# Optimization experiments

Measured on AMD Instinct MI355X. Metric: run time of the kernel, lower is better.

## Reference

```python
import jax, jax.numpy as jnp
import numpy as np

B, N, D_IN, D_HID, D_OUT = 8, 512, 4608, 4608, 1152
DROP = 0.1
INV_SQRT2 = 0.7071067811865476
INV_SQRT_2PI = 0.3989422804014327


def _clean(s):
    # nan -> 1e-5, inf -> 1.0 (matches torch.where chain)
    return jnp.where(jnp.isnan(s), jnp.asarray(1e-5, s.dtype),
                     jnp.where(jnp.isinf(s), jnp.asarray(1.0, s.dtype), s))


def kl_regularizer(w_mu, w_sigma):
    d = w_mu.shape[0]
    ws = jax.nn.softplus(w_sigma)  # log(1+exp(w_sigma))
    return 0.5 * jnp.mean(d * ws + jnp.sum(w_mu * w_mu, axis=0) - d - d * jnp.log(ws))


def vdp_linear(mu_in, Sigma_in, w_mu, w_sigma):
    mu_out = jnp.matmul(mu_in, w_mu)                                 # [B,N,U]
    kl = kl_regularizer(w_mu, w_sigma)
    W_Sigma = jax.nn.softplus(w_sigma)                               # [U]
    Sigma_1 = jnp.matmul(Sigma_in, w_mu * w_mu)                      # w^T Sigma_in w (diag)
    Sigma_2 = jnp.sum(mu_in * mu_in, axis=-1, keepdims=True) * W_Sigma
    Sigma_3 = jnp.sum(Sigma_in, axis=-1, keepdims=True) * W_Sigma
    return mu_out, _clean(Sigma_1 + Sigma_2 + Sigma_3), kl


def vdp_gelu(mu_in, Sigma_in):
    # exact (erf) gelu and its analytic derivative: Phi(x) + x*phi(x)
    cdf = 0.5 * (1.0 + jax.lax.erf(mu_in * INV_SQRT2))
    pdf = jnp.exp(-0.5 * mu_in * mu_in) * INV_SQRT_2PI
    grad = cdf + mu_in * pdf
    return mu_in * cdf, grad * grad * Sigma_in


def vdp_dropout(mu_in, Sigma_in, mask):
    keep = 1.0 - DROP
    m = mask.astype(mu_in.dtype)
    mu_out = mu_in * m / keep                       # torch F.dropout scaling
    Sigma_out = Sigma_in * m / mu_in.shape[-1]      # kept Sigma values (unscaled), / units
    return mu_out, _clean(Sigma_out)


def setup_inputs() -> dict:
    key = jax.random.key(0)
    k = jax.random.split(key, 8)
    mu_in = jax.random.normal(k[0], (B, N, D_IN), dtype=jnp.float32)
    sigma_in = jax.random.uniform(k[1], (B, N, D_IN), dtype=jnp.float32)
    mask1 = jax.random.bernoulli(k[2], 1.0 - DROP, (B, N, D_HID))
    mask2 = jax.random.bernoulli(k[3], 1.0 - DROP, (B, N, D_OUT))
    w_mu1 = 0.05 * jax.random.normal(k[4], (D_IN, D_HID), dtype=jnp.float32)
    w_sigma1 = jnp.full((D_HID,), -4.6, dtype=jnp.float32)
    w_mu2 = 0.05 * jax.random.normal(k[5], (D_HID, D_OUT), dtype=jnp.float32)
    w_sigma2 = jnp.full((D_OUT,), -4.6, dtype=jnp.float32)
    return {"mu_in": mu_in, "sigma_in": sigma_in, "mask1": mask1, "mask2": mask2,
            "w_mu1": w_mu1, "w_sigma1": w_sigma1, "w_mu2": w_mu2, "w_sigma2": w_sigma2}


def reference(mu_in, sigma_in, mask1, mask2, w_mu1, w_sigma1, w_mu2, w_sigma2):
    mu, sig, kl1 = vdp_linear(mu_in, sigma_in, w_mu1, w_sigma1)
    mu, sig = vdp_gelu(mu, sig)
    mu, sig = vdp_dropout(mu, sig, mask1)
    mu, sig, kl2 = vdp_linear(mu, sig, w_mu2, w_sigma2)
    mu, sig = vdp_dropout(mu, sig, mask2)
    return mu, _clean(sig), kl1 + kl2
```

## Files before the change

### kernel.cpp

```cpp
#include <hip/hip_runtime.h>
#include <cstdint>
#include <cstddef>

static constexpr int Mrows = 4096;
static constexpr int K1 = 4608;
static constexpr int N1 = 4608;
static constexpr int N2 = 1152;
static constexpr int SPLITK = 2;
static constexpr int NPART1 = (K1 / 32) * (N1 / 32);
static constexpr int NPART2 = (K1 / 32) * (N2 / 32);

static constexpr float SC_WSQ   = 4096.f;
static constexpr float SC_SIG3  = 16384.f;
static constexpr float DSC_L2   = 1.f / (SC_SIG3 * SC_WSQ);

typedef float  f32x4  __attribute__((ext_vector_type(4)));
typedef __bf16 bf16x8 __attribute__((ext_vector_type(8)));

__device__ __forceinline__ unsigned short f2bf(float f) {
  unsigned int u = __float_as_uint(f);
  u += 0x7fffu + ((u >> 16) & 1u);
  return (unsigned short)(u >> 16);
}
__device__ __forceinline__ float bf2f(unsigned short h) {
  return __uint_as_float(((unsigned int)h) << 16);
}
__device__ __forceinline__ float cleanf(float s) {
  if (__builtin_isnan(s)) return 1e-5f;
  if (__builtin_isinf(s)) return 1.0f;
  return s;
}
__device__ __forceinline__ unsigned int pk_fp8x4(float a, float b, float c, float d) {
  int p = __builtin_amdgcn_cvt_pk_fp8_f32(a, b, 0, false);
  p = __builtin_amdgcn_cvt_pk_fp8_f32(c, d, p, true);
  return (unsigned int)p;
}

__global__ __launch_bounds__(256) void prep_in(
    const float* __restrict__ mu, const float* __restrict__ sg,
    unsigned short* __restrict__ A1, unsigned short* __restrict__ As16,
    float* __restrict__ rmu2, float* __restrict__ rsg)
{
  const int row = blockIdx.x;
  const int tid = threadIdx.x;
  const float4* mup = (const float4*)(mu + (size_t)row * K1);
  const float4* sgp = (const float4*)(sg + (size_t)row * K1);
  ushort4* a1p = (ushort4*)(A1 + (size_t)row * K1);
  ushort4* asp = (ushort4*)(As16 + (size_t)row * K1);
  float smu = 0.f, ssg = 0.f;
  for (int j = tid; j < K1 / 4; j += 256) {
    float4 m4 = mup[j];
    float4 s4 = sgp[j];
    smu += m4.x*m4.x + m4.y*m4.y + m4.z*m4.z + m4.w*m4.w;
    ssg += s4.x + s4.y + s4.z + s4.w;
    a1p[j] = make_ushort4(f2bf(m4.x), f2bf(m4.y), f2bf(m4.z), f2bf(m4.w));
    asp[j] = make_ushort4(f2bf(s4.x), f2bf(s4.y), f2bf(s4.z), f2bf(s4.w));
  }
  __shared__ float red[2][4];
  for (int off = 32; off; off >>= 1) {
    smu += __shfl_down(smu, off);
    ssg += __shfl_down(ssg, off);
  }
  const int lane = tid & 63, wv = tid >> 6;
  if (!lane) { red[0][wv] = smu; red[1][wv] = ssg; }
  __syncthreads();
  if (tid == 0) {
    rmu2[row] = red[0][0] + red[0][1] + red[0][2] + red[0][3];
    rsg[row]  = red[1][0] + red[1][1] + red[1][2] + red[1][3];
  }
}

__global__ __launch_bounds__(256) void prep_w(
    const float* __restrict__ w, unsigned short* __restrict__ Bt,
    void* __restrict__ Bsq, float* __restrict__ partials,
    int K, int N, int sq16)
{
  __shared__ float t[32][33];
  const int kt = blockIdx.x * 32;
  const int nt = blockIdx.y * 32;
  const int tx = threadIdx.x & 31;
  const int ty = threadIdx.x >> 5;
  float loc = 0.f;
#pragma unroll
  for (int i = 0; i < 32; i += 8) {
    float v = w[(size_t)(kt + ty + i) * N + (nt + tx)];
    t[ty + i][tx] = v;
    loc += v * v;
  }
  __syncthreads();
#pragma unroll
  for (int i = 0; i < 32; i += 8) {
    float v = t[tx][ty + i];
    size_t o = (size_t)(nt + ty + i) * K + (kt + tx);
    Bt[o] = f2bf(v);
    if (sq16)
      ((unsigned short*)Bsq)[o] = f2bf(v * v);
    else
      ((unsigned char*)Bsq)[o] =
          (unsigned char)(__builtin_amdgcn_cvt_pk_fp8_f32(v * v * SC_WSQ, 0.f, 0, false) & 0xff);
  }
  __shared__ float red[4];
  for (int off = 32; off; off >>= 1) loc += __shfl_down(loc, off);
  const int lane = threadIdx.x & 63, wv = threadIdx.x >> 6;
  if (!lane) red[wv] = loc;
  __syncthreads();
  if (threadIdx.x == 0)
    partials[blockIdx.y * gridDim.x + blockIdx.x] = red[0] + red[1] + red[2] + red[3];
}

__global__ __launch_bounds__(256) void kl_prep(
    const float* __restrict__ wsig1, const float* __restrict__ wsig2,
    const float* __restrict__ part1, const float* __restrict__ part2,
    float* __restrict__ ws1, float* __restrict__ ws2, float* __restrict__ outkl)
{
  const int tid = threadIdx.x;
  float s1 = 0.f, l1 = 0.f, s2 = 0.f, l2 = 0.f, q1 = 0.f, q2 = 0.f;
  for (int j = tid; j < N1; j += 256) {
    float x = wsig1[j];
    float sp = (x > 20.f) ? x : log1pf(expf(x));
    ws1[j] = sp; s1 += sp; l1 += logf(sp);
  }
  for (int j = tid; j < N2; j += 256) {
    float x = wsig2[j];
    float sp = (x > 20.f) ? x : log1pf(expf(x));
    ws2[j] = sp; s2 += sp; l2 += logf(sp);
  }
  for (int j = tid; j < NPART1; j += 256) q1 += part1[j];
  for (int j = tid; j < NPART2; j += 256) q2 += part2[j];
  __shared__ float red[6][4];
  for (int off = 32; off; off >>= 1) {
    s1 += __shfl_down(s1, off); l1 += __shfl_down(l1, off);
    s2 += __shfl_down(s2, off); l2 += __shfl_down(l2, off);
    q1 += __shfl_down(q1, off); q2 += __shfl_down(q2, off);
  }
  const int lane = tid & 63, wv = tid >> 6;
  if (!lane) {
    red[0][wv] = s1; red[1][wv] = l1; red[2][wv] = s2;
    red[3][wv] = l2; red[4][wv] = q1; red[5][wv] = q2;
  }
  __syncthreads();
  if (tid == 0) {
    float S1v = red[0][0] + red[0][1] + red[0][2] + red[0][3];
    float L1v = red[1][0] + red[1][1] + red[1][2] + red[1][3];
    float S2v = red[2][0] + red[2][1] + red[2][2] + red[2][3];
    float L2v = red[3][0] + red[3][1] + red[3][2] + red[3][3];
    float Q1v = red[4][0] + red[4][1] + red[4][2] + red[4][3];
    float Q2v = red[5][0] + red[5][1] + red[5][2] + red[5][3];
    const float d = 4608.f;
    float kl1 = 0.5f * (d * (S1v / (float)N1) + Q1v / (float)N1 - d - d * (L1v / (float)N1));
    float kl2 = 0.5f * (d * (S2v / (float)N2) + Q2v / (float)N2 - d - d * (L2v / (float)N2));
    outkl[0] = kl1 + kl2;
  }
}

#define GLD16(gp, lp) __builtin_amdgcn_global_load_lds( \
    (__attribute__((address_space(1))) void*)(unsigned short*)(gp), \
    (__attribute__((address_space(3))) void*)(lp), 16, 0, 0)

#define G256_PHASE(I0, STAGE_STMT, TAIL_STMT)                                   \
  {                                                                             \
    bf16x8 Af[2][2];                                                            \
    _Pragma("unroll")                                                           \
    for (int ii = 0; ii < 2; ++ii) {                                            \
      Af[ii][0] = *(const bf16x8*)(cA + (I0 + ii) * 2048 + x0);                 \
      Af[ii][1] = *(const bf16x8*)(cA + (I0 + ii) * 2048 + x1);                 \
    }                                                                           \
    STAGE_STMT;                                                                 \
    __builtin_amdgcn_s_barrier();                                               \
    asm volatile("s_waitcnt lgkmcnt(0)" ::: "memory");                          \
    __builtin_amdgcn_s_setprio(1);                                              \
    _Pragma("unroll")                                                           \
    for (int ii = 0; ii < 2; ++ii)                                              \
      _Pragma("unroll")                                                         \
      for (int j = 0; j < 4; ++j) {                                             \
        acc[I0 + ii][j] = __builtin_amdgcn_mfma_f32_16x16x32_bf16(              \
            Af[ii][0], Bf[j][0], acc[I0 + ii][j], 0, 0, 0);                     \
        acc[I0 + ii][j] = __builtin_amdgcn_mfma_f32_16x16x32_bf16(              \
            Af[ii][1], Bf[j][1], acc[I0 + ii][j], 0, 0, 0);                     \
      }                                                                         \
    __builtin_amdgcn_s_setprio(0);                                              \
    TAIL_STMT;                                                                  \
    __builtin_amdgcn_s_barrier();                                               \
  }

__global__ __launch_bounds__(512, 2) void gemm256(
    const unsigned short* __restrict__ Amu, const unsigned short* __restrict__ Asg,
    const unsigned short* __restrict__ Bmu, const unsigned short* __restrict__ Bsq,
    unsigned short* __restrict__ Cmu, unsigned short* __restrict__ Csg)
{
  __shared__ __align__(16) char smem[131072];
  char* lA = smem;
  char* lB = smem + 65536;

  const int tid  = threadIdx.x;
  const int lane = tid & 63;
  const int wave = tid >> 6;
  const int which = blockIdx.z;
  const unsigned short* Ag = which ? Asg : Amu;
  const unsigned short* Bg = which ? Bsq : Bmu;
  unsigned short* Cg = which ? Csg : Cmu;

  const int m0 = blockIdx.y * 256;
  const int n0 = blockIdx.x * 256;
  const int wm = (wave >> 2) * 128;
  const int wn = (wave & 3) * 64;
  const int fm = lane & 15;
  const int kq = lane >> 4;

  const int rbase = tid >> 3;
  const int gg = (tid & 7) ^ (rbase & 7);
  const unsigned short* gA0 = Ag + (size_t)(m0 + rbase) * K1 + gg * 8;
  const unsigned short* gB0 = Bg + (size_t)(n0 + rbase) * K1 + gg * 8;

  auto stA = [&](int buf, int h, int kt2) {
    const unsigned short* g = gA0 + (size_t)h * 128 * K1 + kt2 * 64;
    char* l = lA + buf * 32768 + h * 16384 + tid * 16;
    GLD16(g, l);
    GLD16(g + (size_t)64 * K1, l + 8192);
  };
  auto stB = [&](int buf, int h, int kt2) {
    const unsigned short* g = gB0 + (size_t)h * 128 * K1 + kt2 * 64;
    char* l = lB + buf * 32768 + h * 16384 + tid * 16;
    GLD16(g, l);
    GLD16(g + (size_t)64 * K1, l + 8192);
  };

  const int ab = (wave >> 2) * 16384 + fm * 128;
  const int bb = ((wave >> 1) & 1) * 16384 + (wave & 1) * 8192 + fm * 128;
  const int x0 = ((0 * 4 + kq) ^ (fm & 7)) * 16;
  const int x1 = ((1 * 4 + kq) ^ (fm & 7)) * 16;

  f32x4 acc[8][4];
#pragma unroll
  for (int i = 0; i < 8; ++i)
#pragma unroll
    for (int j = 0; j < 4; ++j) acc[i][j] = (f32x4){0.f, 0.f, 0.f, 0.f};

  stB(0, 0, 0); stB(0, 1, 0);
  stA(0, 0, 0); stA(0, 1, 0);
  stB(1, 0, 1); stB(1, 1, 1);
  asm volatile("s_waitcnt vmcnt(4)" ::: "memory");
  __builtin_amdgcn_s_barrier();

  const int ksteps = K1 / 64;
  for (int kt = 0; kt < ksteps; ++kt) {
    const int cur = kt & 1;
    const char* cA = lA + cur * 32768 + ab;
    const char* cB = lB + cur * 32768 + bb;

    bf16x8 Bf[4][2];
#pragma unroll
    for (int j = 0; j < 4; ++j) {
      Bf[j][0] = *(const bf16x8*)(cB + j * 2048 + x0);
      Bf[j][1] = *(const bf16x8*)(cB + j * 2048 + x1);
    }

    G256_PHASE(0, if (kt + 1 < ksteps) stA(cur ^ 1, 0, kt + 1), )
    G256_PHASE(2, if (kt + 1 < ksteps) stA(cur ^ 1, 1, kt + 1), )
    G256_PHASE(4, if (kt + 2 < ksteps) stB(cur, 0, kt + 2), )
    G256_PHASE(6, if (kt + 2 < ksteps) stB(cur, 1, kt + 2),
               if (kt < ksteps - 2) asm volatile("s_waitcnt vmcnt(4)" ::: "memory");
               else                 asm volatile("s_waitcnt vmcnt(0)" ::: "memory"))
  }

  const int rr = (lane >> 4) * 4;
  const int cc = lane & 15;
#pragma unroll
  for (int i = 0; i < 8; ++i) {
    const int grow = m0 + wm + i * 16 + rr;
#pragma unroll
    for (int j = 0; j < 4; ++j) {
      const int gcol = n0 + wn + j * 16 + cc;
      unsigned short* cp = Cg + (size_t)grow * N1 + gcol;
#pragma unroll
      for (int r = 0; r < 4; ++r) cp[(size_t)r * N1] = f2bf(acc[i][j][r]);
    }
  }
}

__device__ __forceinline__ void storeC(float v, float* p) { *p = v; }
__device__ __forceinline__ void storeC(float v, unsigned short* p) { *p = f2bf(v); }

template <typename CT>
__global__ __launch_bounds__(256) void gemm_bt2(
    const unsigned short* __restrict__ Aa, const unsigned char* __restrict__ As8,
    const unsigned short* __restrict__ Ba, const unsigned char* __restrict__ Bq8,
    CT* __restrict__ Ca, CT* __restrict__ Cs,
    int M, int N, int Kstride, int Klen, float sdescale)
{
  __shared__ __align__(16) char smem[32768];
  const int tid = threadIdx.x;
  const int lane = tid & 63;
  const int wave = tid >> 6;

  const int which = blockIdx.z & 1;
  const int slice = blockIdx.z >> 1;

  const int m0 = blockIdx.y * 128;
  const int n0 = blockIdx.x * 128;
  const int wm = (wave & 1) * 64;
  const int wn = (wave >> 1) * 64;

  const int fm = lane & 15;
  const int kq = lane >> 4;

  f32x4 acc[4][4];
#pragma unroll
  for (int i = 0; i < 4; i++)
#pragma unroll
    for (int j = 0; j < 4; j++) acc[i][j] = (f32x4){0.f, 0.f, 0.f, 0.f};

  if (which == 0) {
    const unsigned short* A  = Aa + (size_t)slice * Klen;
    const unsigned short* Bt = Ba + (size_t)slice * Klen;
    unsigned short* lA = (unsigned short*)smem;
    unsigned short* lB = (unsigned short*)(smem + 16384);

    const int c0 = tid, c1 = tid + 256;
    const int r0s = c0 >> 2, k0s = (c0 & 3) ^ ((r0s >> 1) & 3);
    const int r1s = c1 >> 2, k1s = (c1 & 3) ^ ((r1s >> 1) & 3);
    const unsigned short* gA0 = A + (size_t)(m0 + r0s) * Kstride + k0s * 8;
    const unsigned short* gA1 = A + (size_t)(m0 + r1s) * Kstride + k1s * 8;
    const unsigned short* gB0 = Bt + (size_t)(n0 + r0s) * Kstride + k0s * 8;
    const unsigned short* gB1 = Bt + (size_t)(n0 + r1s) * Kstride + k1s * 8;

    int aoff[4], boff[4];
#pragma unroll
    for (int i = 0; i < 4; i++) {
      int ra = wm + i * 16 + fm;
      aoff[i] = ra * 32 + ((kq ^ ((ra >> 1) & 3)) * 8);
      int rb = wn + i * 16 + fm;
      boff[i] = rb * 32 + ((kq ^ ((rb >> 1) & 3)) * 8);
    }

    GLD16(gA0, &lA[c0 * 8]); GLD16(gA1, &lA[c1 * 8]);
    GLD16(gB0, &lB[c0 * 8]); GLD16(gB1, &lB[c1 * 8]);
    gA0 += 32; gA1 += 32; gB0 += 32; gB1 += 32;

    const int ksteps = Klen >> 5;
    int cur = 0;
    for (int kt = 0; kt < ksteps; kt++) {
      __syncthreads();
      if (kt + 1 < ksteps) {
        const int nb = cur ^ 1;
        GLD16(gA0, &lA[nb * 4096 + c0 * 8]); GLD16(gA1, &lA[nb * 4096 + c1 * 8]);
        GLD16(gB0, &lB[nb * 4096 + c0 * 8]); GLD16(gB1, &lB[nb * 4096 + c1 * 8]);
        gA0 += 32; gA1 += 32; gB0 += 32; gB1 += 32;
      }
      bf16x8 af[4], bfr[4];
#pragma unroll
      for (int i = 0; i < 4; i++) af[i] = *(const bf16x8*)&lA[cur * 4096 + aoff[i]];
#pragma unroll
      for (int i = 0; i < 4; i++) bfr[i] = *(const bf16x8*)&lB[cur * 4096 + boff[i]];
#pragma unroll
      for (int i = 0; i < 4; i++)
#pragma unroll
        for (int j = 0; j < 4; j++)
          acc[i][j] = __builtin_amdgcn_mfma_f32_16x16x32_bf16(af[i], bfr[j], acc[i][j], 0, 0, 0);
      cur ^= 1;
    }

    CT* C = Ca + (size_t)slice * M * N;
    const int rr = (lane >> 4) * 4;
    const int cc = lane & 15;
#pragma unroll
    for (int i = 0; i < 4; i++) {
      const int grow = m0 + wm + i * 16 + rr;
#pragma unroll
      for (int j = 0; j < 4; j++) {
        const int gcol = n0 + wn + j * 16 + cc;
        CT* cp = C + (size_t)grow * N + gcol;
#pragma unroll
        for (int r = 0; r < 4; r++) storeC(acc[i][j][r], cp + (size_t)r * N);
      }
    }
  } else {
    const unsigned char* A  = As8 + (size_t)slice * Klen;
    const unsigned char* Bt = Bq8 + (size_t)slice * Klen;
    char* lA = smem;
    char* lB = smem + 16384;

    const int s1 = tid, s2 = tid + 256;
    const int r1 = s1 & 127, h1 = s1 >> 7;
    const int r2 = s2 & 127, h2 = s2 >> 7;
    const unsigned char* gA0 = A + (size_t)(m0 + r1) * Kstride + h1 * 16;
    const unsigned char* gA1 = A + (size_t)(m0 + r2) * Kstride + h2 * 16;
    const unsigned char* gB0 = Bt + (size_t)(n0 + r1) * Kstride + h1 * 16;
    const unsigned char* gB1 = Bt + (size_t)(n0 + r2) * Kstride + h2 * 16;

    int aoff8[2][4], boff8[2][4];
#pragma unroll
    for (int hh = 0; hh < 2; hh++)
#pragma unroll
      for (int i = 0; i < 4; i++) {
        const int c = hh * 4 + kq;
        aoff8[hh][i] = (c >> 1) * 2048 + (wm + i * 16 + fm) * 16 + (c & 1) * 8;
        boff8[hh][i] = (c >> 1) * 2048 + (wn + i * 16 + fm) * 16 + (c & 1) * 8;
      }

    GLD16(gA0, lA + s1 * 16); GLD16(gA1, lA + s2 * 16);
    GLD16(gB0, lB + s1 * 16); GLD16(gB1, lB + s2 * 16);
    gA0 += 64; gA1 += 64; gB0 += 64; gB1 += 64;

    const int ksteps = Klen >> 6;
    int cur = 0;
    for (int kt = 0; kt < ksteps; kt++) {
      __syncthreads();
      if (kt + 1 < ksteps) {
        const int nb = cur ^ 1;
        GLD16(gA0, lA + nb * 8192 + s1 * 16); GLD16(gA1, lA + nb * 8192 + s2 * 16);
        GLD16(gB0, lB + nb * 8192 + s1 * 16); GLD16(gB1, lB + nb * 8192 + s2 * 16);
        gA0 += 64; gA1 += 64; gB0 += 64; gB1 += 64;
      }
#pragma unroll
      for (int hh = 0; hh < 2; hh++) {
        long av[4], bv[4];
#pragma unroll
        for (int i = 0; i < 4; i++) av[i] = *(const long*)(lA + cur * 8192 + aoff8[hh][i]);
#pragma unroll
        for (int i = 0; i < 4; i++) bv[i] = *(const long*)(lB + cur * 8192 + boff8[hh][i]);
#pragma unroll
        for (int i = 0; i < 4; i++)
#pragma unroll
          for (int j = 0; j < 4; j++)
            acc[i][j] = __builtin_amdgcn_mfma_f32_16x16x32_fp8_fp8(av[i], bv[j], acc[i][j], 0, 0, 0);
      }
      cur ^= 1;
    }

    CT* C = Cs + (size_t)slice * M * N;
    const int rr = (lane >> 4) * 4;
    const int cc = lane & 15;
#pragma unroll
    for (int i = 0; i < 4; i++) {
      const int grow = m0 + wm + i * 16 + rr;
#pragma unroll
      for (int j = 0; j < 4; j++) {
        const int gcol = n0 + wn + j * 16 + cc;
        CT* cp = C + (size_t)grow * N + gcol;
#pragma unroll
        for (int r = 0; r < 4; r++) storeC(acc[i][j][r] * sdescale, cp + (size_t)r * N);
      }
    }
  }
}

__global__ __launch_bounds__(256) void mid_kernel(
    const unsigned short* __restrict__ mu1, const unsigned short* __restrict__ S1,
    const int* __restrict__ mask1, const float* __restrict__ ws1,
    const float* __restrict__ rmu2, const float* __restrict__ rsg,
    unsigned short* __restrict__ A2, unsigned char* __restrict__ As2,
    float* __restrict__ r2mu, float* __restrict__ r2sg)
{
  const int row = blockIdx.x;
  const int tid = threadIdx.x;
  const float rterm = rmu2[row] + rsg[row];
  const ushort4* mup = (const ushort4*)(mu1 + (size_t)row * N1);
  const ushort4* s1p = (const ushort4*)(S1 + (size_t)row * N1);
  const int4* mkp = (const int4*)(mask1 + (size_t)row * N1);
  const float4* wsp = (const float4*)ws1;
  ushort4* a2p = (ushort4*)(A2 + (size_t)row * N1);
  unsigned int* as2p = (unsigned int*)(As2 + (size_t)row * N1);
  float smu = 0.f, ssg = 0.f;
  for (int j = tid; j < N1 / 4; j += 256) {
    ushort4 m4 = mup[j]; ushort4 s4 = s1p[j]; int4 k4 = mkp[j]; float4 w4 = wsp[j];
    float xv[4] = {bf2f(m4.x), bf2f(m4.y), bf2f(m4.z), bf2f(m4.w)};
    float Sv[4] = {bf2f(s4.x), bf2f(s4.y), bf2f(s4.z), bf2f(s4.w)};
    float wv[4] = {w4.x, w4.y, w4.z, w4.w};
    int   kv[4] = {k4.x, k4.y, k4.z, k4.w};
    unsigned short oa[4];
    float os[4];
#pragma unroll
    for (int t = 0; t < 4; t++) {
      float sig1 = cleanf(Sv[t] + rterm * wv[t]);
      float x = xv[t];
      float cdf = 0.5f * (1.f + erff(x * 0.70710678118654752f));
      float pdf = expf(-0.5f * x * x) * 0.3989422804014327f;
      float g = cdf + x * pdf;
      float mu2v = x * cdf;
      float sig2 = g * g * sig1;
      float mm = (float)kv[t];
      float mu3 = mu2v * mm * (1.f / 0.9f);
      float sig3 = cleanf(sig2 * mm * (1.f / 4608.f));
      smu += mu3 * mu3;
      ssg += sig3;
      oa[t] = f2bf(mu3);
      os[t] = sig3 * SC_SIG3;
    }
    a2p[j] = make_ushort4(oa[0], oa[1], oa[2], oa[3]);
    as2p[j] = pk_fp8x4(os[0], os[1], os[2], os[3]);
  }
  __shared__ float red[2][4];
  for (int off = 32; off; off >>= 1) {
    smu += __shfl_down(smu, off);
    ssg += __shfl_down(ssg, off);
  }
  const int lane = tid & 63, wv2 = tid >> 6;
  if (!lane) { red[0][wv2] = smu; red[1][wv2] = ssg; }
  __syncthreads();
  if (tid == 0) {
    r2mu[row] = red[0][0] + red[0][1] + red[0][2] + red[0][3];
    r2sg[row] = red[1][0] + red[1][1] + red[1][2] + red[1][3];
  }
}

__global__ __launch_bounds__(256) void final_kernel(
    const float* __restrict__ pmu, const float* __restrict__ psig,
    const int* __restrict__ mask2, const float* __restrict__ ws2,
    const float* __restrict__ r2mu, const float* __restrict__ r2sg,
    float* __restrict__ out_mu, float* __restrict__ out_sig)
{
  const int row = blockIdx.x;
  const int tid = threadIdx.x;
  const float rterm = r2mu[row] + r2sg[row];
  const size_t sstride = (size_t)Mrows * N2;
  const float4* mup0 = (const float4*)(pmu + (size_t)row * N2);
  const float4* sbp0 = (const float4*)(psig + (size_t)row * N2);
  const int4* mkp = (const int4*)(mask2 + (size_t)row * N2);
  const float4* wsp = (const float4*)ws2;
  float4* omp = (float4*)(out_mu + (size_t)row * N2);
  float4* osp = (float4*)(out_sig + (size_t)row * N2);
  const size_t s4 = sstride / 4;
  for (int j = tid; j < N2 / 4; j += 256) {
    float4 m4 = mup0[j];
    float4 sb = sbp0[j];
#pragma unroll
    for (int s = 1; s < SPLITK; s++) {
      float4 a = mup0[j + s * s4];
      float4 b = sbp0[j + s * s4];
      m4.x += a.x; m4.y += a.y; m4.z += a.z; m4.w += a.w;
      sb.x += b.x; sb.y += b.y; sb.z += b.z; sb.w += b.w;
    }
    int4 k4 = mkp[j]; float4 w4 = wsp[j];
    float mo[4], so[4];
    float mv[4] = {m4.x, m4.y, m4.z, m4.w};
    float sv[4] = {sb.x, sb.y, sb.z, sb.w};
    float wv[4] = {w4.x, w4.y, w4.z, w4.w};
    int   kv[4] = {k4.x, k4.y, k4.z, k4.w};
#pragma unroll
    for (int t = 0; t < 4; t++) {
      float sig4 = cleanf(sv[t] + rterm * wv[t]);
      float mm = (float)kv[t];
      float mu5 = mv[t] * mm * (1.f / 0.9f);
      float sig5 = cleanf(sig4 * mm * (1.f / 1152.f));
      mo[t] = mu5;
      so[t] = cleanf(sig5);
    }
    omp[j] = make_float4(mo[0], mo[1], mo[2], mo[3]);
    osp[j] = make_float4(so[0], so[1], so[2], so[3]);
  }
}

extern "C" void kernel_launch(void* const* d_in, const int* in_sizes, int n_in,
                              void* d_out, int out_size, void* d_ws, size_t ws_size,
                              hipStream_t stream)
{
  const float* mu_in = (const float*)d_in[0];
  const float* sg_in = (const float*)d_in[1];
  const int* mask1 = (const int*)d_in[2];
  const int* mask2 = (const int*)d_in[3];
  const float* w_mu1 = (const float*)d_in[4];
  const float* wsig1 = (const float*)d_in[5];
  const float* w_mu2 = (const float*)d_in[6];
  const float* wsig2 = (const float*)d_in[7];
  float* out = (float*)d_out;

  char* ws = (char*)d_ws;
  const size_t oA1  = 0;
  const size_t oAs  = oA1  + (size_t)37748736;
  const size_t oB1t = oAs  + (size_t)37748736;
  const size_t oB1q = oB1t + (size_t)42467328;
  const size_t oB2t = oB1q + (size_t)42467328;
  const size_t oB2q = oB2t + (size_t)10616832;
  const size_t oMu1 = oB2q + (size_t)10616832;
  const size_t oS1  = oMu1 + (size_t)37748736;
  const size_t oVec = oS1  + (size_t)37748736;

  unsigned short* A1     = (unsigned short*)(ws + oA1);
  unsigned short* As16   = (unsigned short*)(ws + oAs);
  unsigned char*  As8    = (unsigned char*)(ws + oAs);
  unsigned short* B1t    = (unsigned short*)(ws + oB1t);
  unsigned short* B1sq16 = (unsigned short*)(ws + oB1q);
  unsigned short* B2t    = (unsigned short*)(ws + oB2t);
  unsigned char*  B2q8   = (unsigned char*)(ws + oB2q);
  unsigned short* mu1b   = (unsigned short*)(ws + oMu1);
  unsigned short* S1b16  = (unsigned short*)(ws + oS1);
  float* pmu  = (float*)(ws + oB1t);
  float* psig = (float*)(ws + oMu1);

  float* rmu2 = (float*)(ws + oVec);
  float* rsg  = rmu2 + Mrows;
  float* r2mu = rsg + Mrows;
  float* r2sg = r2mu + Mrows;
  float* ws1v = r2sg + Mrows;
  float* ws2v = ws1v + N1;
  float* part1 = ws2v + N2;
  float* part2 = part1 + NPART1;

  prep_in<<<Mrows, 256, 0, stream>>>(mu_in, sg_in, A1, As16, rmu2, rsg);
  prep_w<<<dim3(K1 / 32, N1 / 32), 256, 0, stream>>>(w_mu1, B1t, (void*)B1sq16, part1, K1, N1, 1);
  prep_w<<<dim3(K1 / 32, N2 / 32), 256, 0, stream>>>(w_mu2, B2t, (void*)B2q8, part2, K1, N2, 0);
  kl_prep<<<1, 256, 0, stream>>>(wsig1, wsig2, part1, part2, ws1v, ws2v,
                                 out + (size_t)2 * Mrows * N2);

  gemm256<<<dim3(N1 / 256, Mrows / 256, 2), 512, 0, stream>>>(
      A1, As16, B1t, B1sq16, mu1b, S1b16);

  mid_kernel<<<Mrows, 256, 0, stream>>>(mu1b, S1b16, mask1, ws1v, rmu2, rsg,
                                        A1, As8, r2mu, r2sg);

  gemm_bt2<float><<<dim3(N2 / 128, Mrows / 128, 2 * SPLITK), 256, 0, stream>>>(
      A1, As8, B2t, B2q8, pmu, psig, Mrows, N2, K1, K1 / SPLITK, DSC_L2);

  final_kernel<<<Mrows, 256, 0, stream>>>(pmu, psig, mask2, ws2v, r2mu, r2sg,
                                          out, out + (size_t)Mrows * N2);
  (void)in_sizes; (void)n_in; (void)out_size; (void)ws_size;
}
```

Baseline: 913.8 us.

## Retile first GEMM to 256x192 blocks with restructured three-phase pipeline

Changes the first big GEMM tile from 256x256 to 256x192, so each wave computes 128x48 and the grid grows from 18 to 24 column blocks (768 CTAs). The point is to get a grid that divides better across the 256 CUs and to use less LDS per block. The k-loop is rebuilt: all 8 A fragments are held in registers, and the MFMA work is split into three barrier-separated phases interleaved with A and B staging. This adds register pressure from holding Af[8][2], and the smaller tile lowers arithmetic intensity.

New measurement: 879.4 us. 1.04x faster.

```diff
diff --git a/kernel.cpp b/kernel.cpp
--- a/kernel.cpp
+++ b/kernel.cpp
@@ -157,38 +157,12 @@
     (__attribute__((address_space(1))) void*)(unsigned short*)(gp), \
     (__attribute__((address_space(3))) void*)(lp), 16, 0, 0)
 
-#define G256_PHASE(I0, STAGE_STMT, TAIL_STMT)                                   \
-  {                                                                             \
-    bf16x8 Af[2][2];                                                            \
-    _Pragma("unroll")                                                           \
-    for (int ii = 0; ii < 2; ++ii) {                                            \
-      Af[ii][0] = *(const bf16x8*)(cA + (I0 + ii) * 2048 + x0);                 \
-      Af[ii][1] = *(const bf16x8*)(cA + (I0 + ii) * 2048 + x1);                 \
-    }                                                                           \
-    STAGE_STMT;                                                                 \
-    __builtin_amdgcn_s_barrier();                                               \
-    asm volatile("s_waitcnt lgkmcnt(0)" ::: "memory");                          \
-    __builtin_amdgcn_s_setprio(1);                                              \
-    _Pragma("unroll")                                                           \
-    for (int ii = 0; ii < 2; ++ii)                                              \
-      _Pragma("unroll")                                                         \
-      for (int j = 0; j < 4; ++j) {                                             \
-        acc[I0 + ii][j] = __builtin_amdgcn_mfma_f32_16x16x32_bf16(              \
-            Af[ii][0], Bf[j][0], acc[I0 + ii][j], 0, 0, 0);                     \
-        acc[I0 + ii][j] = __builtin_amdgcn_mfma_f32_16x16x32_bf16(              \
-            Af[ii][1], Bf[j][1], acc[I0 + ii][j], 0, 0, 0);                     \
-      }                                                                         \
-    __builtin_amdgcn_s_setprio(0);                                              \
-    TAIL_STMT;                                                                  \
-    __builtin_amdgcn_s_barrier();                                               \
-  }
-
 __global__ __launch_bounds__(512, 2) void gemm256(
     const unsigned short* __restrict__ Amu, const unsigned short* __restrict__ Asg,
     const unsigned short* __restrict__ Bmu, const unsigned short* __restrict__ Bsq,
     unsigned short* __restrict__ Cmu, unsigned short* __restrict__ Csg)
 {
-  __shared__ __align__(16) char smem[131072];
+  __shared__ __align__(16) char smem[114688];
   char* lA = smem;
   char* lB = smem + 65536;
 
@@ -201,9 +175,9 @@
   unsigned short* Cg = which ? Csg : Cmu;
 
   const int m0 = blockIdx.y * 256;
-  const int n0 = blockIdx.x * 256;
+  const int n0 = blockIdx.x * 192;
   const int wm = (wave >> 2) * 128;
-  const int wn = (wave & 3) * 64;
+  const int wn = (wave & 3) * 48;
   const int fm = lane & 15;
   const int kq = lane >> 4;
 
@@ -213,54 +187,100 @@
   const unsigned short* gB0 = Bg + (size_t)(n0 + rbase) * K1 + gg * 8;
 
   auto stA = [&](int buf, int h, int kt2) {
-    const unsigned short* g = gA0 + (size_t)h * 128 * K1 + kt2 * 64;
+    const unsigned short* g = gA0 + (size_t)h * 128 * K1 + (size_t)kt2 * 64;
     char* l = lA + buf * 32768 + h * 16384 + tid * 16;
     GLD16(g, l);
     GLD16(g + (size_t)64 * K1, l + 8192);
   };
-  auto stB = [&](int buf, int h, int kt2) {
-    const unsigned short* g = gB0 + (size_t)h * 128 * K1 + kt2 * 64;
-    char* l = lB + buf * 32768 + h * 16384 + tid * 16;
+  auto stB = [&](int buf, int kt2) {
+    const unsigned short* g = gB0 + (size_t)kt2 * 64;
+    char* l = lB + buf * 24576 + tid * 16;
     GLD16(g, l);
     GLD16(g + (size_t)64 * K1, l + 8192);
+    GLD16(g + (size_t)128 * K1, l + 16384);
   };
 
-  const int ab = (wave >> 2) * 16384 + fm * 128;
-  const int bb = ((wave >> 1) & 1) * 16384 + (wave & 1) * 8192 + fm * 128;
+  const int abase = (wm + fm) * 128;
+  const int bbase = 65536 + (wn + fm) * 128;
   const int x0 = ((0 * 4 + kq) ^ (fm & 7)) * 16;
   const int x1 = ((1 * 4 + kq) ^ (fm & 7)) * 16;
 
-  f32x4 acc[8][4];
+  f32x4 acc[8][3];
 #pragma unroll
   for (int i = 0; i < 8; ++i)
 #pragma unroll
-    for (int j = 0; j < 4; ++j) acc[i][j] = (f32x4){0.f, 0.f, 0.f, 0.f};
-
-  stB(0, 0, 0); stB(0, 1, 0);
+    for (int j = 0; j < 3; ++j) acc[i][j] = (f32x4){0.f, 0.f, 0.f, 0.f};
+
+  stB(0, 0);
   stA(0, 0, 0); stA(0, 1, 0);
-  stB(1, 0, 1); stB(1, 1, 1);
-  asm volatile("s_waitcnt vmcnt(4)" ::: "memory");
+  stB(1, 1);
+  asm volatile("s_waitcnt vmcnt(3)" ::: "memory");
   __builtin_amdgcn_s_barrier();
 
   const int ksteps = K1 / 64;
   for (int kt = 0; kt < ksteps; ++kt) {
     const int cur = kt & 1;
-    const char* cA = lA + cur * 32768 + ab;
-    const char* cB = lB + cur * 32768 + bb;
-
-    bf16x8 Bf[4][2];
-#pragma unroll
-    for (int j = 0; j < 4; ++j) {
+    const char* cA = lA + cur * 32768 + abase;
+    const char* cB = smem + cur * 24576 + bbase;
+
+    bf16x8 Af[8][2], Bf[3][2];
+
+#pragma unroll
+    for (int j = 0; j < 3; ++j) {
       Bf[j][0] = *(const bf16x8*)(cB + j * 2048 + x0);
       Bf[j][1] = *(const bf16x8*)(cB + j * 2048 + x1);
     }
-
-    G256_PHASE(0, if (kt + 1 < ksteps) stA(cur ^ 1, 0, kt + 1), )
-    G256_PHASE(2, if (kt + 1 < ksteps) stA(cur ^ 1, 1, kt + 1), )
-    G256_PHASE(4, if (kt + 2 < ksteps) stB(cur, 0, kt + 2), )
-    G256_PHASE(6, if (kt + 2 < ksteps) stB(cur, 1, kt + 2),
-               if (kt < ksteps - 2) asm volatile("s_waitcnt vmcnt(4)" ::: "memory");
-               else                 asm volatile("s_waitcnt vmcnt(0)" ::: "memory"))
+#pragma unroll
+    for (int i = 0; i < 4; ++i) {
+      Af[i][0] = *(const bf16x8*)(cA + i * 2048 + x0);
+      Af[i][1] = *(const bf16x8*)(cA + i * 2048 + x1);
+    }
+    if (kt + 1 < ksteps) stA(cur ^ 1, 0, kt + 1);
+    asm volatile("s_waitcnt lgkmcnt(8)" ::: "memory");
+    __builtin_amdgcn_s_barrier();
+    asm volatile("s_waitcnt lgkmcnt(0)" ::: "memory");
+    __builtin_amdgcn_s_setprio(1);
+#pragma unroll
+    for (int i = 0; i < 4; ++i)
+#pragma unroll
+      for (int j = 0; j < 2; ++j) {
+        acc[i][j] = __builtin_amdgcn_mfma_f32_16x16x32_bf16(Af[i][0], Bf[j][0], acc[i][j], 0, 0, 0);
+        acc[i][j] = __builtin_amdgcn_mfma_f32_16x16x32_bf16(Af[i][1], Bf[j][1], acc[i][j], 0, 0, 0);
+      }
+    __builtin_amdgcn_s_setprio(0);
+    __builtin_amdgcn_s_barrier();
+
+#pragma unroll
+    for (int i = 4; i < 8; ++i) {
+      Af[i][0] = *(const bf16x8*)(cA + i * 2048 + x0);
+      Af[i][1] = *(const bf16x8*)(cA + i * 2048 + x1);
+    }
+    if (kt + 1 < ksteps) stA(cur ^ 1, 1, kt + 1);
+    __builtin_amdgcn_s_barrier();
+    asm volatile("s_waitcnt lgkmcnt(0)" ::: "memory");
+    __builtin_amdgcn_s_setprio(1);
+#pragma unroll
+    for (int i = 4; i < 8; ++i)
+#pragma unroll
+      for (int j = 0; j < 2; ++j) {
+        acc[i][j] = __builtin_amdgcn_mfma_f32_16x16x32_bf16(Af[i][0], Bf[j][0], acc[i][j], 0, 0, 0);
+        acc[i][j] = __builtin_amdgcn_mfma_f32_16x16x32_bf16(Af[i][1], Bf[j][1], acc[i][j], 0, 0, 0);
+      }
+    __builtin_amdgcn_s_setprio(0);
+    __builtin_amdgcn_s_barrier();
+
+    if (kt + 2 < ksteps) stB(cur, kt + 2);
+    __builtin_amdgcn_s_barrier();
+    __builtin_amdgcn_s_setprio(1);
+#pragma unroll
+    for (int i = 0; i < 8; ++i) {
+      acc[i][2] = __builtin_amdgcn_mfma_f32_16x16x32_bf16(Af[i][0], Bf[2][0], acc[i][2], 0, 0, 0);
+      acc[i][2] = __builtin_amdgcn_mfma_f32_16x16x32_bf16(Af[i][1], Bf[2][1], acc[i][2], 0, 0, 0);
+    }
+    __builtin_amdgcn_s_setprio(0);
+    if (kt < ksteps - 2) asm volatile("s_waitcnt vmcnt(3)" ::: "memory");
+    else                 asm volatile("s_waitcnt vmcnt(0)" ::: "memory");
+    __builtin_amdgcn_s_barrier();
   }
 
   const int rr = (lane >> 4) * 4;
@@ -269,7 +289,7 @@
   for (int i = 0; i < 8; ++i) {
     const int grow = m0 + wm + i * 16 + rr;
 #pragma unroll
-    for (int j = 0; j < 4; ++j) {
+    for (int j = 0; j < 3; ++j) {
       const int gcol = n0 + wn + j * 16 + cc;
       unsigned short* cp = Cg + (size_t)grow * N1 + gcol;
 #pragma unroll
@@ -603,7 +623,7 @@
   kl_prep<<<1, 256, 0, stream>>>(wsig1, wsig2, part1, part2, ws1v, ws2v,
                                  out + (size_t)2 * Mrows * N2);
 
-  gemm256<<<dim3(N1 / 256, Mrows / 256, 2), 512, 0, stream>>>(
+  gemm256<<<dim3(N1 / 192, Mrows / 256, 2), 512, 0, stream>>>(
       A1, As16, B1t, B1sq16, mu1b, S1b16);
 
   mid_kernel<<<Mrows, 256, 0, stream>>>(mu1b, S1b16, mask1, ws1v, rmu2, rsg,
```
